# Performance work log

Measured on AMD Instinct MI355X. Metric: run time of the kernel, lower is better.

Reference implementation:

```python
import jax, jax.numpy as jnp
import numpy as np

E = 8192      # number of original edges -> artificial nodes
N = 2048      # number of original graph nodes (id range)
C_IN = 128
C_OUT = 128
NEG_SLOPE = 0.2


def setup_inputs() -> dict:
    key = jax.random.key(0)
    k1, k2, k3, k4, k5 = jax.random.split(key, 5)
    x = jax.random.normal(k1, (E, C_IN), dtype=jnp.float32)
    edge_index = jax.random.randint(k2, (2, E), 0, N, dtype=jnp.int64)
    # GATConv params (heads=1): linear weight, attention vectors, bias
    W = jax.random.normal(k3, (C_IN, C_OUT), dtype=jnp.float32) / np.sqrt(C_IN)
    att_src = jax.random.normal(k4, (C_OUT,), dtype=jnp.float32) / np.sqrt(C_OUT)
    att_dst = jax.random.normal(k5, (C_OUT,), dtype=jnp.float32) / np.sqrt(C_OUT)
    bias = jnp.zeros((C_OUT,), dtype=jnp.float32)
    return {"x": x, "edge_index": edge_index, "W": W,
            "att_src": att_src, "att_dst": att_dst, "bias": bias}


def reference(x, edge_index, W, att_src, att_dst, bias):
    # --- line-graph construction (vectorized version of the O(E^2) loop) ---
    s = edge_index[0]  # [E] source node of each original edge
    d = edge_index[1]  # [E] target node of each original edge
    share = ((s[:, None] == s[None, :]) | (s[:, None] == d[None, :]) |
             (d[:, None] == s[None, :]) | (d[:, None] == d[None, :]))  # [E,E]
    eye = jnp.eye(x.shape[0], dtype=bool)
    # original loop only adds pairs i != j (symmetrically); GATConv then adds self loops
    adj = (share & ~eye) | eye  # adj[i, j]: message j -> i allowed

    # --- GATConv (heads=1, concat) over the dense line-graph adjacency ---
    h = x @ W                       # [E, C_OUT]
    a_src = h @ att_src             # [E] per-source attention logit
    a_dst = h @ att_dst             # [E] per-target attention logit
    scores = a_dst[:, None] + a_src[None, :]          # [E,E], row=target, col=source
    scores = jax.nn.leaky_relu(scores, NEG_SLOPE)
    scores = jnp.where(adj, scores, -jnp.inf)
    alpha = jax.nn.softmax(scores, axis=1)            # softmax over source edges per target
    out = alpha @ h + bias          # [E, C_OUT]
    return out
```

## Files before the change

### kernel.cpp

```cpp
#include <hip/hip_runtime.h>

#define E 8192
#define NNODE 2048
#define C 128
#define CAPN 32
#define NIDX 8
#define NPI (NNODE / NIDX)
#define RPB 16
#define NGEMM (E / RPB)

typedef unsigned int u32;
typedef unsigned long long u64;

__global__ __launch_bounds__(256) void gat_prep(
    const float* __restrict__ x, const float* __restrict__ W,
    const float* __restrict__ att_s, const float* __restrict__ att_d,
    const float* __restrict__ bias, const int* __restrict__ ei,
    float* __restrict__ h, float* __restrict__ asrc, float* __restrict__ adst,
    int* __restrict__ packed, int* __restrict__ cnt, int* __restrict__ nlist)
{
    __shared__ __align__(16) float smem[RPB * C];
    const int tid = threadIdx.x;

    if (blockIdx.x < NIDX) {
        int* lcnt = (int*)smem;
        const int lo = (int)blockIdx.x * NPI;
        if (tid < NPI) lcnt[tid] = 0;
        __syncthreads();
        for (int g = tid; g < E; g += 256) {
            const int s = ei[g], d = ei[E + g];
            if ((g >> 10) == (int)blockIdx.x)
                packed[g] = (s << 16) | d;
            const int sl = s - lo, dl = d - lo;
            if ((unsigned)sl < NPI) {
                const int slot = atomicAdd(&lcnt[sl], 1);
                if (slot < CAPN) nlist[s * CAPN + slot] = g;
            }
            if (d != s && (unsigned)dl < NPI) {
                const int slot = atomicAdd(&lcnt[dl], 1);
                if (slot < CAPN) nlist[d * CAPN + slot] = g;
            }
        }
        __syncthreads();
        if (tid < NPI) cnt[lo + tid] = lcnt[tid];
        return;
    }

    const int lane = tid & 63, wv = tid >> 6;
    const int row0 = ((int)blockIdx.x - NIDX) * RPB;

    {
        const float4* xg = reinterpret_cast<const float4*>(x + (size_t)row0 * C);
        float4* xsv = reinterpret_cast<float4*>(smem);
        xsv[tid]       = xg[tid];
        xsv[tid + 256] = xg[tid + 256];
    }
    __syncthreads();

    float a0x = 0.f, a0y = 0.f, a1x = 0.f, a1y = 0.f;
    float a2x = 0.f, a2y = 0.f, a3x = 0.f, a3y = 0.f;
    const float* xw = smem + (wv * 4) * C;
    const float* Wc = W + 2 * lane;

    #pragma unroll 4
    for (int k4 = 0; k4 < C / 4; ++k4) {
        const float4 v0 = *reinterpret_cast<const float4*>(xw + 0 * C + 4 * k4);
        const float4 v1 = *reinterpret_cast<const float4*>(xw + 1 * C + 4 * k4);
        const float4 v2 = *reinterpret_cast<const float4*>(xw + 2 * C + 4 * k4);
        const float4 v3 = *reinterpret_cast<const float4*>(xw + 3 * C + 4 * k4);
        const float2 w0 = *reinterpret_cast<const float2*>(Wc + (4 * k4 + 0) * C);
        const float2 w1 = *reinterpret_cast<const float2*>(Wc + (4 * k4 + 1) * C);
        const float2 w2 = *reinterpret_cast<const float2*>(Wc + (4 * k4 + 2) * C);
        const float2 w3 = *reinterpret_cast<const float2*>(Wc + (4 * k4 + 3) * C);
#define K4FMA(V, AX, AY)                                        \
        AX = fmaf(V.x, w0.x, AX); AY = fmaf(V.x, w0.y, AY);     \
        AX = fmaf(V.y, w1.x, AX); AY = fmaf(V.y, w1.y, AY);     \
        AX = fmaf(V.z, w2.x, AX); AY = fmaf(V.z, w2.y, AY);     \
        AX = fmaf(V.w, w3.x, AX); AY = fmaf(V.w, w3.y, AY);
        K4FMA(v0, a0x, a0y) K4FMA(v1, a1x, a1y)
        K4FMA(v2, a2x, a2y) K4FMA(v3, a3x, a3y)
#undef K4FMA
    }

    const float2 asv = *reinterpret_cast<const float2*>(att_s + 2 * lane);
    const float2 adv = *reinterpret_cast<const float2*>(att_d + 2 * lane);
    const float2 bv  = *reinterpret_cast<const float2*>(bias  + 2 * lane);
    const int rw0 = row0 + wv * 4;
#define EPI(R, AX, AY) {                                                        \
    *reinterpret_cast<float2*>(&h[(size_t)(rw0 + R) * C + 2 * lane]) =          \
        make_float2(AX + bv.x, AY + bv.y);              \
    float ps = fmaf(AX, asv.x, AY * asv.y);                                     \
    float pd = fmaf(AX, adv.x, AY * adv.y);                                     \
    _Pragma("unroll")                                                           \
    for (int off = 32; off > 0; off >>= 1) {                                    \
        ps += __shfl_xor(ps, off); pd += __shfl_xor(pd, off);                   \
    }                                                                           \
    if (lane == 0) { asrc[rw0 + R] = ps; adst[rw0 + R] = pd; } }
    EPI(0, a0x, a0y) EPI(1, a1x, a1y) EPI(2, a2x, a2y) EPI(3, a3x, a3y)
#undef EPI
}

__global__ __launch_bounds__(256) void gat_aggr(
    const int* __restrict__ packed, const float* __restrict__ h,
    const float* __restrict__ asrc, const float* __restrict__ adst,
    const int* __restrict__ cnt, const int* __restrict__ nlist,
    float* __restrict__ out)
{
    __shared__ float2 lst[4][64];
    const int tid = threadIdx.x, lane = tid & 63, wv = tid >> 6;
    const int i = blockIdx.x * 4 + wv;

    const u32 pi = (u32)packed[i];
    const int si = (int)(pi >> 16), di = (int)(pi & 0xffffu);
    const float adi = adst[i];
    int len_s = cnt[si]; if (len_s > CAPN) len_s = CAPN;
    int len_d = (di == si) ? 0 : cnt[di]; if (len_d > CAPN) len_d = CAPN;
    const int ntot = len_s + len_d;

    int key = 0x7fffffff;
    float sc = -INFINITY;
    bool valid = false;
    if (lane < ntot) {
        const bool from_s = lane < len_s;
        const int j = nlist[(from_s ? si : di) * CAPN + (from_s ? lane : lane - len_s)];
        const u32 pj = (u32)packed[j];
        valid = from_s || ((int)(pj >> 16) != si && (int)(pj & 0xffffu) != si);
        if (valid) {
            const float s0 = adi + asrc[j];
            sc = s0 >= 0.f ? s0 : 0.2f * s0;
            key = j;
        }
    }

    float m = sc;
    #pragma unroll
    for (int off = 32; off > 0; off >>= 1) m = fmaxf(m, __shfl_xor(m, off));
    const int nvalid = (int)__popcll(__ballot(valid));

    float p = __expf(sc - m);

    #pragma unroll
    for (int k = 2; k <= 64; k <<= 1) {
        #pragma unroll
        for (int st = k >> 1; st > 0; st >>= 1) {
            const int   ok = __shfl_xor(key, st);
            const float op = __shfl_xor(p, st);
            const bool takeMin = ((lane & k) == 0) == ((lane & st) == 0);
            if (takeMin ? (ok < key) : (ok > key)) { key = ok; p = op; }
        }
    }
    lst[wv][lane] = make_float2(__int_as_float(key == 0x7fffffff ? i : key), p);

    const int nch = (nvalid + 3) >> 2;
    float lsum = 0.f, o0 = 0.f, o1 = 0.f;
    const float* hb = h + 2 * lane;
    for (int t = 0; t < nch; ++t) {
        const float2 e0 = lst[wv][4 * t + 0];
        const float2 e1 = lst[wv][4 * t + 1];
        const float2 e2 = lst[wv][4 * t + 2];
        const float2 e3 = lst[wv][4 * t + 3];
        const float2 h0 = *reinterpret_cast<const float2*>(hb + (size_t)__float_as_int(e0.x) * C);
        const float2 h1 = *reinterpret_cast<const float2*>(hb + (size_t)__float_as_int(e1.x) * C);
        const float2 h2 = *reinterpret_cast<const float2*>(hb + (size_t)__float_as_int(e2.x) * C);
        const float2 h3 = *reinterpret_cast<const float2*>(hb + (size_t)__float_as_int(e3.x) * C);
        lsum += (e0.y + e1.y) + (e2.y + e3.y);
        o0 = fmaf(e0.y, h0.x, o0); o1 = fmaf(e0.y, h0.y, o1);
        o0 = fmaf(e1.y, h1.x, o0); o1 = fmaf(e1.y, h1.y, o1);
        o0 = fmaf(e2.y, h2.x, o0); o1 = fmaf(e2.y, h2.y, o1);
        o0 = fmaf(e3.y, h3.x, o0); o1 = fmaf(e3.y, h3.y, o1);
    }
    const float inv = 1.0f / lsum;
    *reinterpret_cast<float2*>(&out[(size_t)i * C + 2 * lane]) =
        make_float2(o0 * inv, o1 * inv);
}

extern "C" void kernel_launch(void* const* d_in, const int* in_sizes, int n_in,
                              void* d_out, int out_size, void* d_ws, size_t ws_size,
                              hipStream_t stream) {
    const float* x     = (const float*)d_in[0];
    const int*   ei    = (const int*)d_in[1];
    const float* W     = (const float*)d_in[2];
    const float* att_s = (const float*)d_in[3];
    const float* att_d = (const float*)d_in[4];
    const float* bias  = (const float*)d_in[5];

    float* h      = (float*)d_ws;
    float* asrc   = h + (size_t)E * C;
    float* adst   = asrc + E;
    int*   packed = (int*)(adst + E);
    int*   cnt    = packed + E;
    int*   nlist  = cnt + NNODE;

    gat_prep<<<NIDX + NGEMM, 256, 0, stream>>>(x, W, att_s, att_d, bias, ei,
                                               h, asrc, adst, packed, cnt, nlist);
    gat_aggr<<<E / 4, 256, 0, stream>>>(packed, h, asrc, adst, cnt, nlist,
                                        (float*)d_out);
}
```

Baseline: 47.64 us.

## Spread neighbor-list construction across all GEMM blocks using global atomics

Previously eight dedicated blocks built the node adjacency lists by each scanning all edges with shared-memory atomics, which serialized a long tail. Now each GEMM block handles 256 edges directly with global atomics on cnt, which is zeroed by a memset before the launch. This removes the long-running index blocks but adds a memset launch and global atomic contention. It also makes the GEMM inner loop no longer explicitly unrolled.

```diff
diff --git a/kernel.cpp b/kernel.cpp
--- a/kernel.cpp
+++ b/kernel.cpp
@@ -4,8 +4,6 @@
 #define NNODE 2048
 #define C 128
 #define CAPN 32
-#define NIDX 8
-#define NPI (NNODE / NIDX)
 #define RPB 16
 #define NGEMM (E / RPB)
 
@@ -19,39 +17,24 @@
     float* __restrict__ h, float* __restrict__ asrc, float* __restrict__ adst,
     int* __restrict__ packed, int* __restrict__ cnt, int* __restrict__ nlist)
 {
-    __shared__ __align__(16) float smem[RPB * C];
-    const int tid = threadIdx.x;
-
-    if (blockIdx.x < NIDX) {
-        int* lcnt = (int*)smem;
-        const int lo = (int)blockIdx.x * NPI;
-        if (tid < NPI) lcnt[tid] = 0;
-        __syncthreads();
-        for (int g = tid; g < E; g += 256) {
-            const int s = ei[g], d = ei[E + g];
-            if ((g >> 10) == (int)blockIdx.x)
-                packed[g] = (s << 16) | d;
-            const int sl = s - lo, dl = d - lo;
-            if ((unsigned)sl < NPI) {
-                const int slot = atomicAdd(&lcnt[sl], 1);
-                if (slot < CAPN) nlist[s * CAPN + slot] = g;
-            }
-            if (d != s && (unsigned)dl < NPI) {
-                const int slot = atomicAdd(&lcnt[dl], 1);
-                if (slot < CAPN) nlist[d * CAPN + slot] = g;
-            }
+    const int tid = threadIdx.x, lane = tid & 63, wv = tid >> 6;
+    const int g = blockIdx.x * 256 + tid;
+    if (g < E) {
+        const int s = ei[g], d = ei[E + g];
+        packed[g] = (s << 16) | d;
+        int slot = atomicAdd(&cnt[s], 1);
+        if (slot < CAPN) nlist[s * CAPN + slot] = g;
+        if (d != s) {
+            slot = atomicAdd(&cnt[d], 1);
+            if (slot < CAPN) nlist[d * CAPN + slot] = g;
         }
-        __syncthreads();
-        if (tid < NPI) cnt[lo + tid] = lcnt[tid];
-        return;
     }
 
-    const int lane = tid & 63, wv = tid >> 6;
-    const int row0 = ((int)blockIdx.x - NIDX) * RPB;
-
+    __shared__ __align__(16) float xs[RPB * C];
+    const int row0 = (int)blockIdx.x * RPB;
     {
         const float4* xg = reinterpret_cast<const float4*>(x + (size_t)row0 * C);
-        float4* xsv = reinterpret_cast<float4*>(smem);
+        float4* xsv = reinterpret_cast<float4*>(xs);
         xsv[tid]       = xg[tid];
         xsv[tid + 256] = xg[tid + 256];
     }
@@ -59,28 +42,27 @@
 
     float a0x = 0.f, a0y = 0.f, a1x = 0.f, a1y = 0.f;
     float a2x = 0.f, a2y = 0.f, a3x = 0.f, a3y = 0.f;
-    const float* xw = smem + (wv * 4) * C;
+    const float4* xp0 = reinterpret_cast<const float4*>(xs + (wv * 4 + 0) * C);
+    const float4* xp1 = reinterpret_cast<const float4*>(xs + (wv * 4 + 1) * C);
+    const float4* xp2 = reinterpret_cast<const float4*>(xs + (wv * 4 + 2) * C);
+    const float4* xp3 = reinterpret_cast<const float4*>(xs + (wv * 4 + 3) * C);
     const float* Wc = W + 2 * lane;
 
-    #pragma unroll 4
+#define ROWFMA(V, AX, AY)                                    \
+    AX = fmaf(V.x, w0.x, AX); AY = fmaf(V.x, w0.y, AY);      \
+    AX = fmaf(V.y, w1.x, AX); AY = fmaf(V.y, w1.y, AY);      \
+    AX = fmaf(V.z, w2.x, AX); AY = fmaf(V.z, w2.y, AY);      \
+    AX = fmaf(V.w, w3.x, AX); AY = fmaf(V.w, w3.y, AY);
     for (int k4 = 0; k4 < C / 4; ++k4) {
-        const float4 v0 = *reinterpret_cast<const float4*>(xw + 0 * C + 4 * k4);
-        const float4 v1 = *reinterpret_cast<const float4*>(xw + 1 * C + 4 * k4);
-        const float4 v2 = *reinterpret_cast<const float4*>(xw + 2 * C + 4 * k4);
-        const float4 v3 = *reinterpret_cast<const float4*>(xw + 3 * C + 4 * k4);
+        const float4 v0 = xp0[k4], v1 = xp1[k4], v2 = xp2[k4], v3 = xp3[k4];
         const float2 w0 = *reinterpret_cast<const float2*>(Wc + (4 * k4 + 0) * C);
         const float2 w1 = *reinterpret_cast<const float2*>(Wc + (4 * k4 + 1) * C);
         const float2 w2 = *reinterpret_cast<const float2*>(Wc + (4 * k4 + 2) * C);
         const float2 w3 = *reinterpret_cast<const float2*>(Wc + (4 * k4 + 3) * C);
-#define K4FMA(V, AX, AY)                                        \
-        AX = fmaf(V.x, w0.x, AX); AY = fmaf(V.x, w0.y, AY);     \
-        AX = fmaf(V.y, w1.x, AX); AY = fmaf(V.y, w1.y, AY);     \
-        AX = fmaf(V.z, w2.x, AX); AY = fmaf(V.z, w2.y, AY);     \
-        AX = fmaf(V.w, w3.x, AX); AY = fmaf(V.w, w3.y, AY);
-        K4FMA(v0, a0x, a0y) K4FMA(v1, a1x, a1y)
-        K4FMA(v2, a2x, a2y) K4FMA(v3, a3x, a3y)
-#undef K4FMA
+        ROWFMA(v0, a0x, a0y) ROWFMA(v1, a1x, a1y)
+        ROWFMA(v2, a2x, a2y) ROWFMA(v3, a3x, a3y)
     }
+#undef ROWFMA
 
     const float2 asv = *reinterpret_cast<const float2*>(att_s + 2 * lane);
     const float2 adv = *reinterpret_cast<const float2*>(att_d + 2 * lane);
@@ -191,8 +173,9 @@
     int*   cnt    = packed + E;
     int*   nlist  = cnt + NNODE;
 
-    gat_prep<<<NIDX + NGEMM, 256, 0, stream>>>(x, W, att_s, att_d, bias, ei,
-                                               h, asrc, adst, packed, cnt, nlist);
+    hipMemsetAsync(cnt, 0, NNODE * sizeof(int), stream);
+    gat_prep<<<NGEMM, 256, 0, stream>>>(x, W, att_s, att_d, bias, ei,
+                                        h, asrc, adst, packed, cnt, nlist);
     gat_aggr<<<E / 4, 256, 0, stream>>>(packed, h, asrc, adst, cnt, nlist,
                                         (float*)d_out);
 }
```

Measured after the change: 43.05 us. 1.11x faster.
